# Performance work log

Measured on AMD Instinct MI355X. Metric: run time of the kernel, lower is better.

The kernel has to match this reference:

```python
import jax, jax.numpy as jnp
import numpy as np

B, C, L, D = 16384, 4096, 2, 128  # batch, num_classes, len_label, hidden per prompt slot


def setup_inputs() -> dict:
    key = jax.random.key(0)
    k1, k2 = jax.random.split(key)
    batchs = jax.random.normal(k1, (B, L, D), dtype=jnp.float32)       # masked hidden states
    label2embed = jax.random.normal(k2, (C, L, D), dtype=jnp.float32)  # learned class prompts
    return {"batchs": batchs, "label2embed": label2embed}


def reference(batchs, label2embed):
    # Original ('mm' similarity):
    #   out[b, c] = sum(diag(batchs[b] @ label2embed[c].T))
    #             = sum_{p,d} batchs[b,p,d] * label2embed[c,p,d]
    # Fused row-wise dot product over the flattened (len_label, D) axes,
    # eliminating the O(L^2) mm+diag waste and the B*C Python loop.
    logits = jnp.einsum("bpd,cpd->bc", batchs, label2embed)  # [B, C]
    return logits
```

## Files before the change

kernel.cpp:

```cpp
#include <hip/hip_runtime.h>
#include <hip/hip_bf16.h>
#include <stdint.h>

#define MDIM 16384
#define NDIM 4096
#define KDIM 256

#define BM 128
#define BN 128
#define BK 32

typedef __attribute__((ext_vector_type(8))) short bf16x8;
typedef __attribute__((ext_vector_type(4))) float f32x4;

__device__ __forceinline__ unsigned short f2bf_rne(float f) {
    union { float f; uint32_t u; } v; v.f = f;
    uint32_t u = v.u;
    u += 0x7fffu + ((u >> 16) & 1u);
    return (unsigned short)(u >> 16);
}

__global__ __launch_bounds__(256) void cvt_kernel(const float* __restrict__ a,
                                                  const float* __restrict__ b,
                                                  unsigned short* __restrict__ wa,
                                                  unsigned short* __restrict__ wb) {
    const int64_t nA = (int64_t)MDIM * KDIM;
    int64_t i = ((int64_t)blockIdx.x * 256 + threadIdx.x) * 8;
    const float* src; unsigned short* dst; int64_t off;
    if (i < nA) { src = a; dst = wa; off = i; }
    else        { src = b; dst = wb; off = i - nA; }
    float4 f0 = *(const float4*)(src + off);
    float4 f1 = *(const float4*)(src + off + 4);
    union { unsigned short h[8]; int4 v; } o;
    o.h[0] = f2bf_rne(f0.x); o.h[1] = f2bf_rne(f0.y);
    o.h[2] = f2bf_rne(f0.z); o.h[3] = f2bf_rne(f0.w);
    o.h[4] = f2bf_rne(f1.x); o.h[5] = f2bf_rne(f1.y);
    o.h[6] = f2bf_rne(f1.z); o.h[7] = f2bf_rne(f1.w);
    *(int4*)(dst + off) = o.v;
}

__global__ __launch_bounds__(256) void gemm_bt(const unsigned short* __restrict__ A,
                                               const unsigned short* __restrict__ Bm,
                                               float* __restrict__ out) {
    __shared__ __align__(16) unsigned short sA[BM * BK];
    __shared__ __align__(16) unsigned short sB[BN * BK];

    const int tid  = threadIdx.x;
    const int lane = tid & 63;
    const int wave = tid >> 6;
    const int wm   = wave >> 1;
    const int wn   = wave & 1;
    const int bm   = blockIdx.x >> 5;
    const int bn   = blockIdx.x & 31;

    const unsigned short* Ab = A  + (size_t)bm * BM * KDIM;
    const unsigned short* Bb = Bm + (size_t)bn * BN * KDIM;

    f32x4 acc[4][4] = {};

    const int quad = lane >> 4;
    const int r16  = lane & 15;

    for (int k0 = 0; k0 < KDIM; k0 += BK) {
        __syncthreads();
#pragma unroll
        for (int c = 0; c < 2; ++c) {
            int ch  = tid + c * 256;
            int row = ch >> 2;
            int col = (ch & 3) << 3;
            __builtin_amdgcn_global_load_lds(
                (const __attribute__((address_space(1))) void*)(Ab + (size_t)row * KDIM + k0 + col),
                (__attribute__((address_space(3))) void*)(sA + ch * 8), 16, 0, 0);
            __builtin_amdgcn_global_load_lds(
                (const __attribute__((address_space(1))) void*)(Bb + (size_t)row * KDIM + k0 + col),
                (__attribute__((address_space(3))) void*)(sB + ch * 8), 16, 0, 0);
        }
        __syncthreads();

        bf16x8 af[4], bf[4];
#pragma unroll
        for (int i = 0; i < 4; ++i)
            af[i] = *(const bf16x8*)(sA + ((wm * 64 + i * 16 + r16) * BK + quad * 8));
#pragma unroll
        for (int j = 0; j < 4; ++j)
            bf[j] = *(const bf16x8*)(sB + ((wn * 64 + j * 16 + r16) * BK + quad * 8));

#pragma unroll
        for (int i = 0; i < 4; ++i)
#pragma unroll
            for (int j = 0; j < 4; ++j)
                acc[i][j] = __builtin_amdgcn_mfma_f32_16x16x32_bf16(af[i], bf[j], acc[i][j], 0, 0, 0);
    }

#pragma unroll
    for (int i = 0; i < 4; ++i) {
        int rowb = bm * BM + wm * 64 + i * 16 + quad * 4;
#pragma unroll
        for (int j = 0; j < 4; ++j) {
            int colb = bn * BN + wn * 64 + j * 16 + r16;
            float* p = out + (size_t)rowb * NDIM + colb;
#pragma unroll
            for (int rr = 0; rr < 4; ++rr)
                p[(size_t)rr * NDIM] = acc[i][j][rr];
        }
    }
}

__global__ __launch_bounds__(256) void naive_f32(const float* __restrict__ a,
                                                 const float* __restrict__ b,
                                                 float* __restrict__ out) {
    int64_t idx = (int64_t)blockIdx.x * 256 + threadIdx.x;
    int c = (int)(idx & (NDIM - 1));
    int r = (int)(idx >> 12);
    const float4* ap = (const float4*)(a + (size_t)r * KDIM);
    const float4* bp = (const float4*)(b + (size_t)c * KDIM);
    float s = 0.f;
#pragma unroll 8
    for (int k = 0; k < KDIM / 4; ++k) {
        float4 x = ap[k], y = bp[k];
        s += x.x * y.x + x.y * y.y + x.z * y.z + x.w * y.w;
    }
    out[idx] = s;
}

extern "C" void kernel_launch(void* const* d_in, const int* in_sizes, int n_in,
                              void* d_out, int out_size, void* d_ws, size_t ws_size,
                              hipStream_t stream) {
    const float* a = (const float*)d_in[0];
    const float* b = (const float*)d_in[1];
    float* out = (float*)d_out;

    const size_t need = ((size_t)MDIM + NDIM) * KDIM * sizeof(unsigned short);
    if (d_ws != nullptr && ws_size >= need) {
        unsigned short* wa = (unsigned short*)d_ws;
        unsigned short* wb = wa + (size_t)MDIM * KDIM;
        const int64_t nvec = ((int64_t)MDIM + NDIM) * KDIM / 8;
        cvt_kernel<<<(int)(nvec / 256), 256, 0, stream>>>(a, b, wa, wb);
        gemm_bt<<<(MDIM / BM) * (NDIM / BN), 256, 0, stream>>>(wa, wb, out);
    } else {
        naive_f32<<<(int64_t)MDIM * NDIM / 256, 256, 0, stream>>>(a, b, out);
    }
}
```

Before: 298.7 us.

## Double-buffer LDS tiles in bf16 GEMM and swizzle blocks across XCDs

The GEMM now keeps two shared-memory tile buffers. It issues the global-to-LDS loads for the next K step before computing on the current one, which drops one barrier per iteration and lets load latency overlap with MFMA work. Block indices are remapped so each XCD gets a contiguous band of row tiles, aiming for better L2 reuse of A and B. A minimum-blocks-per-CU hint is added to the launch bounds. Costs: LDS use per block doubles, and the compiler may still insert conservative wait counts that limit the overlap.

```diff
diff --git a/kernel.cpp b/kernel.cpp
--- a/kernel.cpp
+++ b/kernel.cpp
@@ -9,6 +9,7 @@
 #define BM 128
 #define BN 128
 #define BK 32
+#define KSTEPS (KDIM / BK)
 
 typedef __attribute__((ext_vector_type(8))) short bf16x8;
 typedef __attribute__((ext_vector_type(4))) float f32x4;
@@ -39,19 +40,41 @@
     *(int4*)(dst + off) = o.v;
 }
 
-__global__ __launch_bounds__(256) void gemm_bt(const unsigned short* __restrict__ A,
-                                               const unsigned short* __restrict__ Bm,
-                                               float* __restrict__ out) {
-    __shared__ __align__(16) unsigned short sA[BM * BK];
-    __shared__ __align__(16) unsigned short sB[BN * BK];
+__device__ __forceinline__ void stage_tiles(const unsigned short* __restrict__ Ab,
+                                            const unsigned short* __restrict__ Bb,
+                                            unsigned short* sA, unsigned short* sB,
+                                            int tid, int k0) {
+#pragma unroll
+    for (int c = 0; c < 2; ++c) {
+        int ch  = tid + c * 256;
+        int row = ch >> 2;
+        int col = (ch & 3) << 3;
+        __builtin_amdgcn_global_load_lds(
+            (const __attribute__((address_space(1))) void*)(Ab + (size_t)row * KDIM + k0 + col),
+            (__attribute__((address_space(3))) void*)(sA + ch * 8), 16, 0, 0);
+        __builtin_amdgcn_global_load_lds(
+            (const __attribute__((address_space(1))) void*)(Bb + (size_t)row * KDIM + k0 + col),
+            (__attribute__((address_space(3))) void*)(sB + ch * 8), 16, 0, 0);
+    }
+}
+
+__global__ __launch_bounds__(256, 4) void gemm_bt(const unsigned short* __restrict__ A,
+                                                  const unsigned short* __restrict__ Bm,
+                                                  float* __restrict__ out) {
+    __shared__ __align__(16) unsigned short sA[2][BM * BK];
+    __shared__ __align__(16) unsigned short sB[2][BN * BK];
 
     const int tid  = threadIdx.x;
     const int lane = tid & 63;
     const int wave = tid >> 6;
     const int wm   = wave >> 1;
     const int wn   = wave & 1;
-    const int bm   = blockIdx.x >> 5;
-    const int bn   = blockIdx.x & 31;
+
+    const int id  = blockIdx.x;
+    const int xcd = id & 7;
+    const int g   = id >> 3;
+    const int bm  = (xcd << 4) | (g >> 5);
+    const int bn  = g & 31;
 
     const unsigned short* Ab = A  + (size_t)bm * BM * KDIM;
     const unsigned short* Bb = Bm + (size_t)bn * BN * KDIM;
@@ -61,29 +84,24 @@
     const int quad = lane >> 4;
     const int r16  = lane & 15;
 
-    for (int k0 = 0; k0 < KDIM; k0 += BK) {
+    stage_tiles(Ab, Bb, sA[0], sB[0], tid, 0);
+
+#pragma unroll
+    for (int step = 0; step < KSTEPS; ++step) {
         __syncthreads();
-#pragma unroll
-        for (int c = 0; c < 2; ++c) {
-            int ch  = tid + c * 256;
-            int row = ch >> 2;
-            int col = (ch & 3) << 3;
-            __builtin_amdgcn_global_load_lds(
-                (const __attribute__((address_space(1))) void*)(Ab + (size_t)row * KDIM + k0 + col),
-                (__attribute__((address_space(3))) void*)(sA + ch * 8), 16, 0, 0);
-            __builtin_amdgcn_global_load_lds(
-                (const __attribute__((address_space(1))) void*)(Bb + (size_t)row * KDIM + k0 + col),
-                (__attribute__((address_space(3))) void*)(sB + ch * 8), 16, 0, 0);
-        }
-        __syncthreads();
+        if (step + 1 < KSTEPS)
+            stage_tiles(Ab, Bb, sA[(step + 1) & 1], sB[(step + 1) & 1], tid, (step + 1) * BK);
+
+        const unsigned short* cA = sA[step & 1];
+        const unsigned short* cB = sB[step & 1];
 
         bf16x8 af[4], bf[4];
 #pragma unroll
         for (int i = 0; i < 4; ++i)
-            af[i] = *(const bf16x8*)(sA + ((wm * 64 + i * 16 + r16) * BK + quad * 8));
+            af[i] = *(const bf16x8*)(cA + ((wm * 64 + i * 16 + r16) * BK + quad * 8));
 #pragma unroll
         for (int j = 0; j < 4; ++j)
-            bf[j] = *(const bf16x8*)(sB + ((wn * 64 + j * 16 + r16) * BK + quad * 8));
+            bf[j] = *(const bf16x8*)(cB + ((wn * 64 + j * 16 + r16) * BK + quad * 8));
 
 #pragma unroll
         for (int i = 0; i < 4; ++i)
```

New measurement: 295.5 us. About the same (-1.1%).
